# Performance work log

Hardware: AMD Instinct MI355X
Metric: run time of the kernel (lower is better)

The kernel has to match this reference:

```python
import jax, jax.numpy as jnp
import numpy as np

B, T, C, H = 4, 1024, 1024, 16
HS = C // H  # head_size = 64
EPS = 1e-5


def layer_norm(x, w, b):
    mu = jnp.mean(x, axis=-1, keepdims=True)
    var = jnp.mean(jnp.square(x - mu), axis=-1, keepdims=True)
    return (x - mu) * jax.lax.rsqrt(var + EPS) * w + b


def setup_inputs() -> dict:
    key = jax.random.key(0)
    ks = jax.random.split(key, 12)
    s = 0.02
    return {
        "x": jax.random.normal(ks[0], (B, T, C), jnp.float32),
        "ln1_w": jnp.ones((C,), jnp.float32),
        "ln1_b": jnp.zeros((C,), jnp.float32),
        "Wk": jax.random.normal(ks[1], (H, C, HS), jnp.float32) * s,
        "Wq": jax.random.normal(ks[2], (H, C, HS), jnp.float32) * s,
        "Wv": jax.random.normal(ks[3], (H, C, HS), jnp.float32) * s,
        "Wo": jax.random.normal(ks[4], (C, C), jnp.float32) * s,
        "bo": jnp.zeros((C,), jnp.float32),
        "ln2_w": jnp.ones((C,), jnp.float32),
        "ln2_b": jnp.zeros((C,), jnp.float32),
        "W1": jax.random.normal(ks[5], (C, 4 * C), jnp.float32) * s,
        "b1": jnp.zeros((4 * C,), jnp.float32),
        "prelu_a": jnp.asarray(0.25, jnp.float32),
        "W2": jax.random.normal(ks[6], (4 * C, C), jnp.float32) * s,
        "b2": jnp.zeros((C,), jnp.float32),
    }


def reference(x, ln1_w, ln1_b, Wk, Wq, Wv, Wo, bo, ln2_w, ln2_b, W1, b1, prelu_a, W2, b2):
    # --- self-attention branch (pre-LN) ---
    h = layer_norm(x, ln1_w, ln1_b)  # [B,T,C]
    k = jnp.einsum('btc,hcd->bhtd', h, Wk)
    q = jnp.einsum('btc,hcd->bhtd', h, Wq)
    v = jnp.einsum('btc,hcd->bhtd', h, Wv)
    # NOTE: source computes k @ q^T (not q @ k^T) scaled by n_embd**-0.5
    wei = jnp.einsum('bhtd,bhsd->bhts', k, q) * (C ** -0.5)  # [B,H,T,T]
    causal = jnp.tril(jnp.ones((T, T), bool))
    wei = jnp.where(causal, wei, -jnp.inf)
    wei = jax.nn.softmax(wei, axis=-1)
    out = jnp.einsum('bhts,bhsd->bthd', wei, v).reshape(B, T, C)
    out = out @ Wo + bo
    x = x + out
    # --- feed-forward branch (pre-LN) ---
    h2 = layer_norm(x, ln2_w, ln2_b)
    f = h2 @ W1 + b1
    f = jnp.where(f > 0, f, prelu_a * f)  # PReLU, single scalar param
    f = f @ W2 + b2
    return x + f
```

## Files before the change

### kernel.cpp

```cpp
#include <hip/hip_runtime.h>


typedef __bf16 bf16_t;
typedef __attribute__((ext_vector_type(8))) __bf16 bfx8;
typedef __attribute__((ext_vector_type(4))) __bf16 bfx4;
typedef __attribute__((ext_vector_type(4))) float f32x4;
typedef __attribute__((ext_vector_type(8))) unsigned short u16x8;
typedef unsigned int u32;

#define MFMA_BF16(a, b, c) __builtin_amdgcn_mfma_f32_16x16x32_bf16((a), (b), (c), 0, 0, 0)
#define GLOAD_LDS16(g, l)                                                     \
  __builtin_amdgcn_global_load_lds((__attribute__((address_space(1))) void*)(g), \
                                   (__attribute__((address_space(3))) void*)(l), 16, 0, 0)
#define SBAR() __builtin_amdgcn_sched_barrier(0)
#define VMW(N)                                          \
  asm volatile("s_waitcnt vmcnt(" #N ")" ::: "memory"); \
  __builtin_amdgcn_sched_barrier(0)

__device__ __forceinline__ int xcd_swz(int wg, int nb) {
  return (wg & 7) * (nb >> 3) + (wg >> 3);
}

__global__ __launch_bounds__(256) void ln_kernel(const float* __restrict__ x,
                                                 const float* __restrict__ w,
                                                 const float* __restrict__ b,
                                                 bf16_t* __restrict__ out) {
  const int row = blockIdx.x;
  const int tid = threadIdx.x;
  const float4 v = reinterpret_cast<const float4*>(x + (size_t)row * 1024)[tid];
  float s = v.x + v.y + v.z + v.w;
  float s2 = v.x * v.x + v.y * v.y + v.z * v.z + v.w * v.w;
#pragma unroll
  for (int off = 1; off < 64; off <<= 1) {
    s += __shfl_xor(s, off);
    s2 += __shfl_xor(s2, off);
  }
  __shared__ float red[8];
  const int wv = tid >> 6;
  if ((tid & 63) == 0) {
    red[wv] = s;
    red[4 + wv] = s2;
  }
  __syncthreads();
  s = red[0] + red[1] + red[2] + red[3];
  s2 = red[4] + red[5] + red[6] + red[7];
  const float mu = s * (1.0f / 1024.0f);
  const float rs = rsqrtf(s2 * (1.0f / 1024.0f) - mu * mu + 1e-5f);
  const float4 wv4 = reinterpret_cast<const float4*>(w)[tid];
  const float4 bv4 = reinterpret_cast<const float4*>(b)[tid];
  bfx4 o;
  o[0] = (bf16_t)((v.x - mu) * rs * wv4.x + bv4.x);
  o[1] = (bf16_t)((v.y - mu) * rs * wv4.y + bv4.y);
  o[2] = (bf16_t)((v.z - mu) * rs * wv4.z + bv4.z);
  o[3] = (bf16_t)((v.w - mu) * rs * wv4.w + bv4.w);
  reinterpret_cast<bfx4*>(out + (size_t)row * 1024)[tid] = o;
}

__device__ __forceinline__ void tc_body(const float* __restrict__ in,
                                        bf16_t* __restrict__ out, int K, int N, int k0,
                                        int n0, float (*tile)[65], int t) {
  const int rl = t >> 4, cl = (t & 15) * 4;
#pragma unroll
  for (int p = 0; p < 4; ++p) {
    const int r = p * 16 + rl;
    const float4 v = *reinterpret_cast<const float4*>(in + (size_t)(k0 + r) * N + n0 + cl);
    tile[r][cl] = v.x;
    tile[r][cl + 1] = v.y;
    tile[r][cl + 2] = v.z;
    tile[r][cl + 3] = v.w;
  }
  __syncthreads();
#pragma unroll
  for (int p = 0; p < 2; ++p) {
    const int idx = p * 256 + t;
    const int n = idx >> 3, kc = (idx & 7) * 8;
    bfx8 o;
#pragma unroll
    for (int i = 0; i < 8; ++i) o[i] = (bf16_t)tile[kc + i][n];
    *reinterpret_cast<bfx8*>(out + (size_t)(n0 + n) * K + k0 + kc) = o;
  }
}

__global__ __launch_bounds__(256) void transpose_cast(const float* __restrict__ in,
                                                      bf16_t* __restrict__ out, int K,
                                                      int N) {
  __shared__ float tile[64][65];
  tc_body(in, out, K, N, blockIdx.x * 64, blockIdx.y * 64, tile, threadIdx.x);
}

__global__ __launch_bounds__(256) void transpose_qkv(const float* __restrict__ Wq,
                                                     const float* __restrict__ Wk,
                                                     const float* __restrict__ Wv,
                                                     bf16_t* __restrict__ out) {
  __shared__ float tile[64][65];
  const int z = blockIdx.y;
  const int sel = z >> 4, h = z & 15;
  const float* in = ((sel == 0) ? Wq : (sel == 1) ? Wk : Wv) + h * 65536;
  bf16_t* o = out + (size_t)sel * 1048576 + h * 65536;
  tc_body(in, o, 1024, 64, blockIdx.x * 64, 0, tile, threadIdx.x);
}

enum { EPI_QKV = 0, EPI_WO = 1 };

template <int EPI, int BM, int BN, int NT>
__global__ __launch_bounds__(NT, 2) void gemm_bt(
    const bf16_t* __restrict__ A, const bf16_t* __restrict__ BT,
    const float* __restrict__ bias, const float* __restrict__ res,
    float* __restrict__ outf, bf16_t* __restrict__ ob0, bf16_t* __restrict__ ob1,
    bf16_t* __restrict__ ob2, int K, int N) {
  constexpr int WM = 2;
  constexpr int WN = NT / 64 / WM;
  constexpr int MF = BM / WM / 16;
  constexpr int NF = BN / WN / 16;
  constexpr int ACH = BM * 64 / (NT * 8);
  constexpr int BCH = BN * 64 / (NT * 8);
  constexpr int LOADS = ACH + BCH;
  static_assert(LOADS == 8 || LOADS == 6, "add a vmcnt case");
  __shared__ __align__(16) bf16_t sA[2][BM * 64];
  __shared__ __align__(16) bf16_t sB[2][BN * 64];
  const int tid = threadIdx.x;
  const int lane = tid & 63;
  const int w = tid >> 6;
  const int wr = w / WN, wc = w % WN;
  const int g = lane >> 4, l15 = lane & 15;
  const int nb = gridDim.x * gridDim.y;
  const int wg = blockIdx.y * gridDim.x + blockIdx.x;
  const int sg = xcd_swz(wg, nb);
  const int bx = sg % gridDim.x, by = sg / gridDim.x;
  const int row0 = bx * BM, col0 = by * BN;
  const int rowbase = row0 + wr * (BM / WM);
  const int colbase = wc * (BN / WN);

  f32x4 acc[MF][NF] = {};

  auto stage = [&](int k0, int buf) {
#pragma unroll
    for (int j = 0; j < ACH; ++j) {
      const int chunk = j * NT + tid;
      const int r = chunk >> 3, c = chunk & 7;
      GLOAD_LDS16(A + (size_t)(row0 + r) * K + k0 + ((c ^ (r & 7)) * 8),
                  sA[buf] + chunk * 8);
    }
#pragma unroll
    for (int j = 0; j < BCH; ++j) {
      const int chunk = j * NT + tid;
      const int r = chunk >> 3, c = chunk & 7;
      GLOAD_LDS16(BT + (size_t)(col0 + r) * K + k0 + ((c ^ (r & 7)) * 8),
                  sB[buf] + chunk * 8);
    }
  };

  stage(0, 0);
  const int nk = K >> 6;
  for (int t = 0; t < nk; ++t) {
    const int cur = t & 1;
    if (t + 1 < nk) {
      stage((t + 1) << 6, cur ^ 1);
      SBAR();
      if constexpr (LOADS == 8)
        asm volatile("s_waitcnt vmcnt(8)" ::: "memory");
      else
        asm volatile("s_waitcnt vmcnt(6)" ::: "memory");
    } else {
      SBAR();
      asm volatile("s_waitcnt vmcnt(0)" ::: "memory");
    }
    __builtin_amdgcn_s_barrier();
    SBAR();
    const bf16_t* __restrict__ pA = sA[cur];
    const bf16_t* __restrict__ pB = sB[cur];
#pragma unroll
    for (int kk = 0; kk < 2; ++kk) {
      bfx8 af[MF], bfr[NF];
#pragma unroll
      for (int m = 0; m < MF; ++m) {
        const int r = wr * (BM / WM) + m * 16 + l15;
        const int c = (kk * 4 + g) ^ (r & 7);
        af[m] = *reinterpret_cast<const bfx8*>(pA + r * 64 + c * 8);
      }
#pragma unroll
      for (int n = 0; n < NF; ++n) {
        const int r = colbase + n * 16 + l15;
        const int c = (kk * 4 + g) ^ (r & 7);
        bfr[n] = *reinterpret_cast<const bfx8*>(pB + r * 64 + c * 8);
      }
#pragma unroll
      for (int m = 0; m < MF; ++m)
#pragma unroll
        for (int n = 0; n < NF; ++n) acc[m][n] = MFMA_BF16(af[m], bfr[n], acc[m][n]);
    }
    SBAR();
    __builtin_amdgcn_s_barrier();
  }

#pragma unroll
  for (int m = 0; m < MF; ++m) {
#pragma unroll
    for (int n = 0; n < NF; ++n) {
#pragma unroll
      for (int j = 0; j < 4; ++j) {
        const int row = rowbase + m * 16 + (g << 2) + j;
        const int col = col0 + colbase + n * 16 + l15;
        const float v = acc[m][n][j];
        if (EPI == EPI_QKV) {
          const int sel = col >> 10;
          const int h = (col >> 6) & 15, d = col & 63;
          const int bb = row >> 10, t = row & 1023;
          bf16_t* dst = (sel == 0) ? ob0 : (sel == 1) ? ob1 : ob2;
          dst[((size_t)(bb * 16 + h) * 1024 + t) * 64 + d] = (bf16_t)v;
        } else {
          outf[(size_t)row * N + col] = v + bias[col] + res[(size_t)row * N + col];
        }
      }
    }
  }
}

__device__ __forceinline__ void stageA8(const bf16_t* __restrict__ A, int Ks, int row0,
                                        int k0, int mh, bf16_t* dst, int tid) {
#pragma unroll
  for (int g2 = 0; g2 < 2; ++g2) {
    const int band = g2 * 128 + mh * 64;
    const int row = band + (tid >> 3);
    GLOAD_LDS16(A + (size_t)(row0 + row) * Ks + k0 + (((tid & 7) ^ (row & 7)) * 8),
                dst + band * 64 + tid * 8);
  }
}

__device__ __forceinline__ void stageB8(const bf16_t* __restrict__ BT, int Ks, int col0,
                                        int k0, int nh, bf16_t* dst, int tid) {
#pragma unroll
  for (int g2 = 0; g2 < 2; ++g2) {
    const int rho = g2 * 64 + (tid >> 3);
    const int grow = (rho >> 5) * 64 + nh * 32 + (rho & 31);
    GLOAD_LDS16(BT + (size_t)(col0 + grow) * Ks + k0 + (((tid & 7) ^ (rho & 7)) * 8),
                dst + nh * 8192 + g2 * 4096 + tid * 8);
  }
}

template <int MH>
__device__ __forceinline__ void read_a8(const bf16_t* __restrict__ pA, int wr, int l15,
                                        int g, bfx8 (&af)[4][2]) {
#pragma unroll
  for (int i = 0; i < 4; ++i) {
    const int r = wr * 128 + (MH * 4 + i) * 16 + l15;
#pragma unroll
    for (int kk = 0; kk < 2; ++kk)
      af[i][kk] =
          *reinterpret_cast<const bfx8*>(pA + r * 64 + (((kk * 4 + g) ^ (r & 7)) * 8));
  }
}

template <int NH>
__device__ __forceinline__ void read_b8(const bf16_t* __restrict__ pB, int wc, int l15,
                                        int g, bfx8 (&bf)[2][2]) {
#pragma unroll
  for (int i = 0; i < 2; ++i) {
    const int rho = wc * 32 + i * 16 + l15;
#pragma unroll
    for (int kk = 0; kk < 2; ++kk)
      bf[i][kk] = *reinterpret_cast<const bfx8*>(pB + NH * 8192 + rho * 64 +
                                                 (((kk * 4 + g) ^ (rho & 7)) * 8));
  }
}

template <int MH, int NH>
__device__ __forceinline__ void mma16(const bfx8 (&af)[4][2], const bfx8 (&bf)[2][2],
                                      f32x4 (&acc)[8][4]) {
  __builtin_amdgcn_s_setprio(1);
#pragma unroll
  for (int i = 0; i < 4; ++i)
#pragma unroll
    for (int jn = 0; jn < 2; ++jn)
#pragma unroll
      for (int kk = 0; kk < 2; ++kk)
        acc[MH * 4 + i][NH * 2 + jn] =
            MFMA_BF16(af[i][kk], bf[jn][kk], acc[MH * 4 + i][NH * 2 + jn]);
  __builtin_amdgcn_s_setprio(0);
}

#define PHX(READS, STAGE, WAITC, MMA)                   \
  {                                                     \
    READS;                                              \
    STAGE;                                              \
    WAITC;                                              \
    __builtin_amdgcn_s_barrier();                       \
    asm volatile("s_waitcnt lgkmcnt(0)" ::: "memory");  \
    SBAR();                                             \
    MMA;                                                \
    SBAR();                                             \
    __builtin_amdgcn_s_barrier();                       \
  }

template <bool PRELU>
__global__ __launch_bounds__(512, 1) void gemm_8ph(
    const bf16_t* __restrict__ A, const bf16_t* __restrict__ BT,
    const float* __restrict__ bias, const float* __restrict__ prelu,
    bf16_t* __restrict__ outb, int Ks, int Klen, int N, size_t zstride, int nx,
    int nxy) {
  __shared__ __align__(16) bf16_t sA[2][256 * 64];
  __shared__ __align__(16) bf16_t sB[2][256 * 64];
  const int tid = threadIdx.x;
  const int lane = tid & 63;
  const int w = tid >> 6;
  const int wr = w >> 2, wc = w & 3;
  const int g = lane >> 4, l15 = lane & 15;
  const int sg = xcd_swz(blockIdx.x, gridDim.x);
  const int bz = sg / nxy;
  const int rxy = sg - bz * nxy;
  const int by = rxy / nx, bx = rxy - by * nx;
  const int row0 = bx * 256, col0 = by * 256;
  const int koff = bz * Klen;

  f32x4 acc[8][4] = {};
  bfx8 af[4][2];
  bfx8 b0[2][2], b1[2][2];

  stageA8(A, Ks, row0, koff, 0, sA[0], tid);
  stageB8(BT, Ks, col0, koff, 0, sB[0], tid);
  stageB8(BT, Ks, col0, koff, 1, sB[0], tid);
  stageA8(A, Ks, row0, koff, 1, sA[0], tid);
  stageA8(A, Ks, row0, koff + 64, 0, sA[1], tid);
  stageB8(BT, Ks, col0, koff + 64, 0, sB[1], tid);
  VMW(4);
  __builtin_amdgcn_s_barrier();

  const int nt = Klen >> 7;
  for (int j = 0; j < nt; ++j) {
    const bool more = (j + 1 < nt);
    const int ku1 = koff + ((2 * j + 1) << 6);
    const int k2 = koff + ((2 * j + 2) << 6);
    const int k3 = koff + ((2 * j + 3) << 6);
    PHX((read_a8<0>(sA[0], wr, l15, g, af), read_b8<0>(sB[0], wc, l15, g, b0)),
        stageB8(BT, Ks, col0, ku1, 1, sB[1], tid), ,
        (mma16<0, 0>(af, b0, acc)));
    PHX((read_b8<1>(sB[0], wc, l15, g, b1)),
        stageA8(A, Ks, row0, ku1, 1, sA[1], tid), ,
        (mma16<0, 1>(af, b1, acc)));
    PHX((read_a8<1>(sA[0], wr, l15, g, af)),
        if (more) stageA8(A, Ks, row0, k2, 0, sA[0], tid), ,
        (mma16<1, 0>(af, b0, acc)));
    PHX(, if (more) stageB8(BT, Ks, col0, k2, 0, sB[0], tid),
        if (more) { VMW(4); } else { VMW(0); },
        (mma16<1, 1>(af, b1, acc)));
    PHX((read_a8<0>(sA[1], wr, l15, g, af), read_b8<0>(sB[1], wc, l15, g, b0)),
        if (more) stageB8(BT, Ks, col0, k2, 1, sB[0], tid), ,
        (mma16<0, 0>(af, b0, acc)));
    PHX((read_b8<1>(sB[1], wc, l15, g, b1)),
        if (more) stageA8(A, Ks, row0, k2, 1, sA[0], tid), ,
        (mma16<0, 1>(af, b1, acc)));
    PHX((read_a8<1>(sA[1], wr, l15, g, af)),
        if (more) stageA8(A, Ks, row0, k3, 0, sA[1], tid), ,
        (mma16<1, 0>(af, b0, acc)));
    PHX(, if (more) stageB8(BT, Ks, col0, k3, 0, sB[1], tid),
        if (more) { VMW(4); },
        (mma16<1, 1>(af, b1, acc)));
  }

  bf16_t* o = outb + (size_t)bz * zstride;
  const float pa = PRELU ? prelu[0] : 0.0f;
#pragma unroll
  for (int m = 0; m < 8; ++m) {
#pragma unroll
    for (int n = 0; n < 4; ++n) {
#pragma unroll
      for (int j = 0; j < 4; ++j) {
        const int row = row0 + wr * 128 + m * 16 + (g << 2) + j;
        const int col = col0 + wc * 64 + n * 16 + l15;
        float t = acc[m][n][j];
        if (PRELU) {
          t += bias[col];
          t = (t > 0.0f) ? t : pa * t;
        }
        o[(size_t)row * N + col] = (bf16_t)t;
      }
    }
  }
}

__global__ __launch_bounds__(256) void reduce_mlp2(const bf16_t* __restrict__ part,
                                                   const float* __restrict__ b2,
                                                   float* __restrict__ out) {
  const int idx = (blockIdx.x * 256 + threadIdx.x) * 8;
  const int col = idx & 1023;
  float a[8];
  {
    const float4 o0 = *reinterpret_cast<const float4*>(out + idx);
    const float4 o1 = *reinterpret_cast<const float4*>(out + idx + 4);
    const float4 b0 = *reinterpret_cast<const float4*>(b2 + col);
    const float4 b1 = *reinterpret_cast<const float4*>(b2 + col + 4);
    a[0] = o0.x + b0.x; a[1] = o0.y + b0.y; a[2] = o0.z + b0.z; a[3] = o0.w + b0.w;
    a[4] = o1.x + b1.x; a[5] = o1.y + b1.y; a[6] = o1.z + b1.z; a[7] = o1.w + b1.w;
  }
#pragma unroll
  for (int s = 0; s < 4; ++s) {
    const u16x8 p = *reinterpret_cast<const u16x8*>(part + (size_t)s * 4194304 + idx);
#pragma unroll
    for (int i = 0; i < 8; ++i) a[i] += __uint_as_float((u32)p[i] << 16);
  }
  float4 r0{a[0], a[1], a[2], a[3]}, r1{a[4], a[5], a[6], a[7]};
  *reinterpret_cast<float4*>(out + idx) = r0;
  *reinterpret_cast<float4*>(out + idx + 4) = r1;
}

__global__ __launch_bounds__(256) void attn_kernel(const bf16_t* __restrict__ kproj,
                                                   const bf16_t* __restrict__ qproj,
                                                   const bf16_t* __restrict__ vproj,
                                                   bf16_t* __restrict__ att) {
  __shared__ __align__(16) bf16_t sK[2][64 * 64];
  __shared__ __align__(16) bf16_t sVt[2][64 * 64];
  __shared__ __align__(16) bf16_t sP[4][16 * 64];
  const int tid = threadIdx.x, lane = tid & 63, w = tid >> 6;
  const int g = lane >> 4, l15 = lane & 15;
  const int f = blockIdx.x;
  const int tb = 15 - ((f >> 3) >> 3);
  const int bh = (((f >> 3) & 7) << 3) + (f & 7);
  const size_t head = (size_t)bh * (1024 * 64);
  const int b = bh >> 4, h = bh & 15;
  const int vrow = 2 * (tid >> 3);
  const int vdb = tid & 7;
  const int t0 = tb * 64;
  const int nsb = tb + 1;

  bfx8 aq0, aq1;
  {
    const bf16_t* qrow = kproj + head + (size_t)(t0 + w * 16 + l15) * 64 + g * 8;
    aq0 = *reinterpret_cast<const bfx8*>(qrow);
    aq1 = *reinterpret_cast<const bfx8*>(qrow + 32);
  }

  {
#pragma unroll
    for (int j = 0; j < 2; ++j) {
      const int chunk = j * 256 + tid;
      const int r = chunk >> 3, c = chunk & 7;
      const int cs = c ^ (r & 7);
      GLOAD_LDS16(qproj + head + (size_t)r * 64 + cs * 8, sK[0] + chunk * 8);
    }
    const bf16_t* vp = vproj + head + (size_t)vrow * 64 + vdb * 8;
    const u16x8 v0 = *reinterpret_cast<const u16x8*>(vp);
    const u16x8 v1 = *reinterpret_cast<const u16x8*>(vp + 64);
#pragma unroll
    for (int i = 0; i < 8; ++i) {
      const int d = vdb * 8 + i;
      const int cc = ((vrow >> 3) ^ i ^ vdb) & 7;
      const u32 pk = ((u32)v1[i] << 16) | (u32)v0[i];
      *reinterpret_cast<u32*>(sVt[0] + d * 64 + cc * 8 + (vrow & 7)) = pk;
    }
  }
  __syncthreads();

  f32x4 accO[4] = {};
  float m2[4], lp[4];
#pragma unroll
  for (int j = 0; j < 4; ++j) {
    m2[j] = -1e30f;
    lp[j] = 0.0f;
  }

  for (int sb = 0; sb < nsb; ++sb) {
    const int cur = sb & 1;
    const bool pf = (sb + 1 < nsb);
    const bool diag = (sb == tb);
    u16x8 v0n, v1n;
    if (pf) {
      const int s0n = (sb + 1) * 64;
#pragma unroll
      for (int j = 0; j < 2; ++j) {
        const int chunk = j * 256 + tid;
        const int r = chunk >> 3, c = chunk & 7;
        const int cs = c ^ (r & 7);
        GLOAD_LDS16(qproj + head + (size_t)(s0n + r) * 64 + cs * 8, sK[cur ^ 1] + chunk * 8);
      }
      const bf16_t* vp = vproj + head + (size_t)(s0n + vrow) * 64 + vdb * 8;
      v0n = *reinterpret_cast<const u16x8*>(vp);
      v1n = *reinterpret_cast<const u16x8*>(vp + 64);
    }

    f32x4 accS[4] = {};
    const bf16_t* sKc = sK[cur];
#pragma unroll
    for (int kk = 0; kk < 2; ++kk) {
      const bfx8 aq = kk ? aq1 : aq0;
#pragma unroll
      for (int n = 0; n < 4; ++n) {
        const int r = n * 16 + l15;
        const int c = (kk * 4 + g) ^ (r & 7);
        const bfx8 bk = *reinterpret_cast<const bfx8*>(sKc + r * 64 + c * 8);
        accS[n] = MFMA_BF16(aq, bk, accS[n]);
      }
    }

    constexpr float SC = 0.04508056640625f;
    const int rbase = t0 + w * 16 + (g << 2);
    const int cbase = sb * 64 + l15;
    float rmx[4];
    float dmax = -3e38f;
#pragma unroll
    for (int j = 0; j < 4; ++j) {
      const int t = rbase + j;
      float mx = -1e30f;
      if (diag) {
#pragma unroll
        for (int n = 0; n < 4; ++n) {
          float v = accS[n][j] * SC;
          v = ((cbase + n * 16) <= t) ? v : -1e30f;
          accS[n][j] = v;
          mx = fmaxf(mx, v);
        }
      } else {
#pragma unroll
        for (int n = 0; n < 4; ++n) {
          const float v = accS[n][j] * SC;
          accS[n][j] = v;
          mx = fmaxf(mx, v);
        }
      }
      rmx[j] = mx;
      dmax = fmaxf(dmax, mx - m2[j]);
    }
    if (__any(dmax > 8.0f)) {
#pragma unroll
      for (int j = 0; j < 4; ++j) {
        float mx = rmx[j];
        mx = fmaxf(mx, __shfl_xor(mx, 1));
        mx = fmaxf(mx, __shfl_xor(mx, 2));
        mx = fmaxf(mx, __shfl_xor(mx, 4));
        mx = fmaxf(mx, __shfl_xor(mx, 8));
        const float mnew = fmaxf(m2[j], mx);
        const float al = __builtin_amdgcn_exp2f(m2[j] - mnew);
        m2[j] = mnew;
        lp[j] *= al;
#pragma unroll
        for (int n = 0; n < 4; ++n) accO[n][j] *= al;
      }
    }
#pragma unroll
    for (int j = 0; j < 4; ++j) {
      float s = 0.0f;
#pragma unroll
      for (int n = 0; n < 4; ++n) {
        const float p = __builtin_amdgcn_exp2f(accS[n][j] - m2[j]);
        accS[n][j] = p;
        s += p;
      }
      lp[j] += s;
    }

    bf16_t* sPw = sP[w];
#pragma unroll
    for (int n = 0; n < 4; ++n)
#pragma unroll
      for (int j = 0; j < 4; ++j) {
        const int r = (g << 2) + j;
        const int s = n * 16 + l15;
        const int cc = (s >> 3) ^ (r & 7);
        sPw[r * 64 + cc * 8 + (s & 7)] = (bf16_t)accS[n][j];
      }

    const bf16_t* sVc = sVt[cur];
#pragma unroll
    for (int kk = 0; kk < 2; ++kk) {
      bfx8 ap;
      {
        const int r = l15;
        const int c = (kk * 4 + g) ^ (r & 7);
        ap = *reinterpret_cast<const bfx8*>(sPw + r * 64 + c * 8);
      }
#pragma unroll
      for (int n = 0; n < 4; ++n) {
        const int d = n * 16 + l15;
        const int c = (kk * 4 + g) ^ (d & 7) ^ ((d >> 3) & 7);
        const bfx8 bv = *reinterpret_cast<const bfx8*>(sVc + d * 64 + c * 8);
        accO[n] = MFMA_BF16(ap, bv, accO[n]);
      }
    }

    if (pf) {
#pragma unroll
      for (int i = 0; i < 8; ++i) {
        const int d = vdb * 8 + i;
        const int cc = ((vrow >> 3) ^ i ^ vdb) & 7;
        const u32 pk = ((u32)v1n[i] << 16) | (u32)v0n[i];
        *reinterpret_cast<u32*>(sVt[cur ^ 1] + d * 64 + cc * 8 + (vrow & 7)) = pk;
      }
    }
    __syncthreads();
  }

#pragma unroll
  for (int j = 0; j < 4; ++j) {
    float l = lp[j];
    l += __shfl_xor(l, 1);
    l += __shfl_xor(l, 2);
    l += __shfl_xor(l, 4);
    l += __shfl_xor(l, 8);
    const float inv = 1.0f / l;
    const int t = t0 + w * 16 + (g << 2) + j;
#pragma unroll
    for (int n = 0; n < 4; ++n) {
      const int d = n * 16 + l15;
      att[((size_t)(b * 1024 + t)) * 1024 + h * 64 + d] = (bf16_t)(accO[n][j] * inv);
    }
  }
}

extern "C" void kernel_launch(void* const* d_in, const int* in_sizes, int n_in,
                              void* d_out, int out_size, void* d_ws, size_t ws_size,
                              hipStream_t stream) {
  (void)in_sizes; (void)n_in; (void)out_size; (void)ws_size;
  const float* x = (const float*)d_in[0];
  const float* ln1w = (const float*)d_in[1];
  const float* ln1b = (const float*)d_in[2];
  const float* Wk = (const float*)d_in[3];
  const float* Wq = (const float*)d_in[4];
  const float* Wv = (const float*)d_in[5];
  const float* Wo = (const float*)d_in[6];
  const float* bo = (const float*)d_in[7];
  const float* ln2w = (const float*)d_in[8];
  const float* ln2b = (const float*)d_in[9];
  const float* W1 = (const float*)d_in[10];
  const float* b1 = (const float*)d_in[11];
  const float* pa = (const float*)d_in[12];
  const float* W2 = (const float*)d_in[13];
  const float* b2 = (const float*)d_in[14];
  float* out = (float*)d_out;
  char* ws = (char*)d_ws;
  const size_t MB = 1ull << 20;
  bf16_t* h1 = (bf16_t*)(ws + 0 * MB);
  bf16_t* h2 = (bf16_t*)(ws + 8 * MB);
  bf16_t* qb = (bf16_t*)(ws + 16 * MB);
  bf16_t* kb = (bf16_t*)(ws + 24 * MB);
  bf16_t* vb = (bf16_t*)(ws + 32 * MB);
  bf16_t* attb = (bf16_t*)(ws + 40 * MB);
  bf16_t* fbuf = (bf16_t*)(ws + 48 * MB);
  bf16_t* part = (bf16_t*)(ws + 16 * MB);
  bf16_t* WqkvT = (bf16_t*)(ws + 80 * MB);
  bf16_t* WoT = (bf16_t*)(ws + 86 * MB);
  bf16_t* W1T = (bf16_t*)(ws + 88 * MB);
  bf16_t* W2T = (bf16_t*)(ws + 96 * MB);

  transpose_qkv<<<dim3(16, 48), 256, 0, stream>>>(Wq, Wk, Wv, WqkvT);
  transpose_cast<<<dim3(16, 16), 256, 0, stream>>>(Wo, WoT, 1024, 1024);
  transpose_cast<<<dim3(16, 64), 256, 0, stream>>>(W1, W1T, 1024, 4096);
  transpose_cast<<<dim3(64, 16), 256, 0, stream>>>(W2, W2T, 4096, 1024);

  ln_kernel<<<4096, 256, 0, stream>>>(x, ln1w, ln1b, h1);
  gemm_bt<EPI_QKV, 256, 256, 512><<<dim3(16, 12), 512, 0, stream>>>(
      h1, WqkvT, nullptr, nullptr, nullptr, qb, kb, vb, 1024, 3072);
  attn_kernel<<<1024, 256, 0, stream>>>(kb, qb, vb, attb);
  gemm_bt<EPI_WO, 64, 128, 256><<<dim3(64, 8), 256, 0, stream>>>(
      attb, WoT, bo, x, out, nullptr, nullptr, nullptr, 1024, 1024);
  ln_kernel<<<4096, 256, 0, stream>>>(out, ln2w, ln2b, h2);
  gemm_8ph<true><<<256, 512, 0, stream>>>(h2, W1T, b1, pa, fbuf, 1024, 1024, 4096, 0, 16,
                                          256);
  gemm_8ph<false><<<256, 512, 0, stream>>>(fbuf, W2T, nullptr, nullptr, part, 4096, 1024,
                                           1024, 4194304, 16, 64);
  reduce_mlp2<<<2048, 256, 0, stream>>>(part, b2, out);
}
```

Measured before the change: 203.4 us.

## Widen attention blocks to 128 queries and replace split-K MLP2 with single GEMM

The attention kernel now runs 512-thread blocks covering 128 query rows (8 waves), with the two 64-row halves sharing each K/V tile load. Waves whose row tile is already finished skip the compute for extra key blocks. This cuts redundant K/V loads and the block count, at the cost of idle waves on the diagonal block. The second MLP GEMM drops the split-K bf16 partial sums and separate reduce kernel. It uses gemm_bt with the EPI_WO epilogue, adding bias and residual in place, which removes a launch and the partial-buffer traffic but gives less parallelism for K=4096.

Measured after the change: 216.3 us. +6.3%, slower.

```diff
diff --git a/kernel.cpp b/kernel.cpp
--- a/kernel.cpp
+++ b/kernel.cpp
@@ -378,49 +378,25 @@
   }
 }
 
-__global__ __launch_bounds__(256) void reduce_mlp2(const bf16_t* __restrict__ part,
-                                                   const float* __restrict__ b2,
-                                                   float* __restrict__ out) {
-  const int idx = (blockIdx.x * 256 + threadIdx.x) * 8;
-  const int col = idx & 1023;
-  float a[8];
-  {
-    const float4 o0 = *reinterpret_cast<const float4*>(out + idx);
-    const float4 o1 = *reinterpret_cast<const float4*>(out + idx + 4);
-    const float4 b0 = *reinterpret_cast<const float4*>(b2 + col);
-    const float4 b1 = *reinterpret_cast<const float4*>(b2 + col + 4);
-    a[0] = o0.x + b0.x; a[1] = o0.y + b0.y; a[2] = o0.z + b0.z; a[3] = o0.w + b0.w;
-    a[4] = o1.x + b1.x; a[5] = o1.y + b1.y; a[6] = o1.z + b1.z; a[7] = o1.w + b1.w;
-  }
-#pragma unroll
-  for (int s = 0; s < 4; ++s) {
-    const u16x8 p = *reinterpret_cast<const u16x8*>(part + (size_t)s * 4194304 + idx);
-#pragma unroll
-    for (int i = 0; i < 8; ++i) a[i] += __uint_as_float((u32)p[i] << 16);
-  }
-  float4 r0{a[0], a[1], a[2], a[3]}, r1{a[4], a[5], a[6], a[7]};
-  *reinterpret_cast<float4*>(out + idx) = r0;
-  *reinterpret_cast<float4*>(out + idx + 4) = r1;
-}
-
-__global__ __launch_bounds__(256) void attn_kernel(const bf16_t* __restrict__ kproj,
+__global__ __launch_bounds__(512) void attn_kernel(const bf16_t* __restrict__ kproj,
                                                    const bf16_t* __restrict__ qproj,
                                                    const bf16_t* __restrict__ vproj,
                                                    bf16_t* __restrict__ att) {
   __shared__ __align__(16) bf16_t sK[2][64 * 64];
   __shared__ __align__(16) bf16_t sVt[2][64 * 64];
-  __shared__ __align__(16) bf16_t sP[4][16 * 64];
+  __shared__ __align__(16) bf16_t sP[8][16 * 64];
   const int tid = threadIdx.x, lane = tid & 63, w = tid >> 6;
   const int g = lane >> 4, l15 = lane & 15;
   const int f = blockIdx.x;
-  const int tb = 15 - ((f >> 3) >> 3);
-  const int bh = (((f >> 3) & 7) << 3) + (f & 7);
+  const int p = 7 - (f >> 6);
+  const int bh = f & 63;
   const size_t head = (size_t)bh * (1024 * 64);
   const int b = bh >> 4, h = bh & 15;
-  const int vrow = 2 * (tid >> 3);
+  const int vrow = tid >> 3;
   const int vdb = tid & 7;
-  const int t0 = tb * 64;
-  const int nsb = tb + 1;
+  const int t0 = p * 128;
+  const int nsb = 2 * p + 2;
+  const int wtb = 2 * p + (w >> 2);
 
   bfx8 aq0, aq1;
   {
@@ -430,22 +406,15 @@
   }
 
   {
-#pragma unroll
-    for (int j = 0; j < 2; ++j) {
-      const int chunk = j * 256 + tid;
-      const int r = chunk >> 3, c = chunk & 7;
-      const int cs = c ^ (r & 7);
-      GLOAD_LDS16(qproj + head + (size_t)r * 64 + cs * 8, sK[0] + chunk * 8);
-    }
-    const bf16_t* vp = vproj + head + (size_t)vrow * 64 + vdb * 8;
-    const u16x8 v0 = *reinterpret_cast<const u16x8*>(vp);
-    const u16x8 v1 = *reinterpret_cast<const u16x8*>(vp + 64);
+    const int r = tid >> 3, c = tid & 7;
+    GLOAD_LDS16(qproj + head + (size_t)r * 64 + ((c ^ (r & 7)) * 8), sK[0] + tid * 8);
+    const bfx8 v0 =
+        *reinterpret_cast<const bfx8*>(vproj + head + (size_t)vrow * 64 + vdb * 8);
 #pragma unroll
     for (int i = 0; i < 8; ++i) {
       const int d = vdb * 8 + i;
       const int cc = ((vrow >> 3) ^ i ^ vdb) & 7;
-      const u32 pk = ((u32)v1[i] << 16) | (u32)v0[i];
-      *reinterpret_cast<u32*>(sVt[0] + d * 64 + cc * 8 + (vrow & 7)) = pk;
+      sVt[0][d * 64 + cc * 8 + (vrow & 7)] = v0[i];
     }
   }
   __syncthreads();
@@ -461,118 +430,115 @@
   for (int sb = 0; sb < nsb; ++sb) {
     const int cur = sb & 1;
     const bool pf = (sb + 1 < nsb);
-    const bool diag = (sb == tb);
-    u16x8 v0n, v1n;
+    bfx8 v0n;
     if (pf) {
       const int s0n = (sb + 1) * 64;
-#pragma unroll
-      for (int j = 0; j < 2; ++j) {
-        const int chunk = j * 256 + tid;
-        const int r = chunk >> 3, c = chunk & 7;
-        const int cs = c ^ (r & 7);
-        GLOAD_LDS16(qproj + head + (size_t)(s0n + r) * 64 + cs * 8, sK[cur ^ 1] + chunk * 8);
-      }
-      const bf16_t* vp = vproj + head + (size_t)(s0n + vrow) * 64 + vdb * 8;
-      v0n = *reinterpret_cast<const u16x8*>(vp);
-      v1n = *reinterpret_cast<const u16x8*>(vp + 64);
-    }
-
-    f32x4 accS[4] = {};
-    const bf16_t* sKc = sK[cur];
-#pragma unroll
-    for (int kk = 0; kk < 2; ++kk) {
-      const bfx8 aq = kk ? aq1 : aq0;
-#pragma unroll
-      for (int n = 0; n < 4; ++n) {
-        const int r = n * 16 + l15;
-        const int c = (kk * 4 + g) ^ (r & 7);
-        const bfx8 bk = *reinterpret_cast<const bfx8*>(sKc + r * 64 + c * 8);
-        accS[n] = MFMA_BF16(aq, bk, accS[n]);
-      }
-    }
-
-    constexpr float SC = 0.04508056640625f;
-    const int rbase = t0 + w * 16 + (g << 2);
-    const int cbase = sb * 64 + l15;
-    float rmx[4];
-    float dmax = -3e38f;
-#pragma unroll
-    for (int j = 0; j < 4; ++j) {
-      const int t = rbase + j;
-      float mx = -1e30f;
-      if (diag) {
+      const int r = tid >> 3, c = tid & 7;
+      GLOAD_LDS16(qproj + head + (size_t)(s0n + r) * 64 + ((c ^ (r & 7)) * 8),
+                  sK[cur ^ 1] + tid * 8);
+      v0n = *reinterpret_cast<const bfx8*>(vproj + head + (size_t)(s0n + vrow) * 64 +
+                                           vdb * 8);
+    }
+
+    if (sb <= wtb) {
+      const bool diag = (sb == wtb);
+      f32x4 accS[4] = {};
+      const bf16_t* sKc = sK[cur];
+#pragma unroll
+      for (int kk = 0; kk < 2; ++kk) {
+        const bfx8 aq = kk ? aq1 : aq0;
 #pragma unroll
         for (int n = 0; n < 4; ++n) {
-          float v = accS[n][j] * SC;
-          v = ((cbase + n * 16) <= t) ? v : -1e30f;
-          accS[n][j] = v;
-          mx = fmaxf(mx, v);
-        }
-      } else {
+          const int r = n * 16 + l15;
+          const int c = (kk * 4 + g) ^ (r & 7);
+          const bfx8 bk = *reinterpret_cast<const bfx8*>(sKc + r * 64 + c * 8);
+          accS[n] = MFMA_BF16(aq, bk, accS[n]);
+        }
+      }
+
+      constexpr float SC = 0.04508056640625f;
+      const int rbase = t0 + w * 16 + (g << 2);
+      const int cbase = sb * 64 + l15;
+      float rmx[4];
+      float dmax = -3e38f;
+#pragma unroll
+      for (int j = 0; j < 4; ++j) {
+        const int t = rbase + j;
+        float mx = -1e30f;
+        if (diag) {
+#pragma unroll
+          for (int n = 0; n < 4; ++n) {
+            float v = accS[n][j] * SC;
+            v = ((cbase + n * 16) <= t) ? v : -1e30f;
+            accS[n][j] = v;
+            mx = fmaxf(mx, v);
+          }
+        } else {
+#pragma unroll
+          for (int n = 0; n < 4; ++n) {
+            const float v = accS[n][j] * SC;
+            accS[n][j] = v;
+            mx = fmaxf(mx, v);
+          }
+        }
+        rmx[j] = mx;
+        dmax = fmaxf(dmax, mx - m2[j]);
+      }
+      if (__any(dmax > 8.0f)) {
+#pragma unroll
+        for (int j = 0; j < 4; ++j) {
+          float mx = rmx[j];
+          mx = fmaxf(mx, __shfl_xor(mx, 1));
+          mx = fmaxf(mx, __shfl_xor(mx, 2));
+          mx = fmaxf(mx, __shfl_xor(mx, 4));
+          mx = fmaxf(mx, __shfl_xor(mx, 8));
+          const float mnew = fmaxf(m2[j], mx);
+          const float al = __builtin_amdgcn_exp2f(m2[j] - mnew);
+          m2[j] = mnew;
+          lp[j] *= al;
+#pragma unroll
+          for (int n = 0; n < 4; ++n) accO[n][j] *= al;
+        }
+      }
+#pragma unroll
+      for (int j = 0; j < 4; ++j) {
+        float s = 0.0f;
 #pragma unroll
         for (int n = 0; n < 4; ++n) {
-          const float v = accS[n][j] * SC;
-          accS[n][j] = v;
-          mx = fmaxf(mx, v);
-        }
-      }
-      rmx[j] = mx;
-      dmax = fmaxf(dmax, mx - m2[j]);
-    }
-    if (__any(dmax > 8.0f)) {
-#pragma unroll
-      for (int j = 0; j < 4; ++j) {
-        float mx = rmx[j];
-        mx = fmaxf(mx, __shfl_xor(mx, 1));
-        mx = fmaxf(mx, __shfl_xor(mx, 2));
-        mx = fmaxf(mx, __shfl_xor(mx, 4));
-        mx = fmaxf(mx, __shfl_xor(mx, 8));
-        const float mnew = fmaxf(m2[j], mx);
-        const float al = __builtin_amdgcn_exp2f(m2[j] - mnew);
-        m2[j] = mnew;
-        lp[j] *= al;
-#pragma unroll
-        for (int n = 0; n < 4; ++n) accO[n][j] *= al;
-      }
-    }
-#pragma unroll
-    for (int j = 0; j < 4; ++j) {
-      float s = 0.0f;
-#pragma unroll
-      for (int n = 0; n < 4; ++n) {
-        const float p = __builtin_amdgcn_exp2f(accS[n][j] - m2[j]);
-        accS[n][j] = p;
-        s += p;
-      }
-      lp[j] += s;
-    }
-
-    bf16_t* sPw = sP[w];
-#pragma unroll
-    for (int n = 0; n < 4; ++n)
-#pragma unroll
-      for (int j = 0; j < 4; ++j) {
-        const int r = (g << 2) + j;
-        const int s = n * 16 + l15;
-        const int cc = (s >> 3) ^ (r & 7);
-        sPw[r * 64 + cc * 8 + (s & 7)] = (bf16_t)accS[n][j];
-      }
-
-    const bf16_t* sVc = sVt[cur];
-#pragma unroll
-    for (int kk = 0; kk < 2; ++kk) {
-      bfx8 ap;
-      {
-        const int r = l15;
-        const int c = (kk * 4 + g) ^ (r & 7);
-        ap = *reinterpret_cast<const bfx8*>(sPw + r * 64 + c * 8);
-      }
-#pragma unroll
-      for (int n = 0; n < 4; ++n) {
-        const int d = n * 16 + l15;
-        const int c = (kk * 4 + g) ^ (d & 7) ^ ((d >> 3) & 7);
-        const bfx8 bv = *reinterpret_cast<const bfx8*>(sVc + d * 64 + c * 8);
-        accO[n] = MFMA_BF16(ap, bv, accO[n]);
+          const float pv = __builtin_amdgcn_exp2f(accS[n][j] - m2[j]);
+          accS[n][j] = pv;
+          s += pv;
+        }
+        lp[j] += s;
+      }
+
+      bf16_t* sPw = sP[w];
+#pragma unroll
+      for (int n = 0; n < 4; ++n)
+#pragma unroll
+        for (int j = 0; j < 4; ++j) {
+          const int r = (g << 2) + j;
+          const int s = n * 16 + l15;
+          const int cc = (s >> 3) ^ (r & 7);
+          sPw[r * 64 + cc * 8 + (s & 7)] = (bf16_t)accS[n][j];
+        }
+
+      const bf16_t* sVc = sVt[cur];
+#pragma unroll
+      for (int kk = 0; kk < 2; ++kk) {
+        bfx8 ap;
+        {
+          const int r = l15;
+          const int c = (kk * 4 + g) ^ (r & 7);
+          ap = *reinterpret_cast<const bfx8*>(sPw + r * 64 + c * 8);
+        }
+#pragma unroll
+        for (int n = 0; n < 4; ++n) {
+          const int d = n * 16 + l15;
+          const int c = (kk * 4 + g) ^ (d & 7) ^ ((d >> 3) & 7);
+          const bfx8 bv = *reinterpret_cast<const bfx8*>(sVc + d * 64 + c * 8);
+          accO[n] = MFMA_BF16(ap, bv, accO[n]);
+        }
       }
     }
 
@@ -581,8 +547,7 @@
       for (int i = 0; i < 8; ++i) {
         const int d = vdb * 8 + i;
         const int cc = ((vrow >> 3) ^ i ^ vdb) & 7;
-        const u32 pk = ((u32)v1n[i] << 16) | (u32)v0n[i];
-        *reinterpret_cast<u32*>(sVt[cur ^ 1] + d * 64 + cc * 8 + (vrow & 7)) = pk;
+        sVt[cur ^ 1][d * 64 + cc * 8 + (vrow & 7)] = v0n[i];
       }
     }
     __syncthreads();
@@ -634,7 +599,6 @@
   bf16_t* vb = (bf16_t*)(ws + 32 * MB);
   bf16_t* attb = (bf16_t*)(ws + 40 * MB);
   bf16_t* fbuf = (bf16_t*)(ws + 48 * MB);
-  bf16_t* part = (bf16_t*)(ws + 16 * MB);
   bf16_t* WqkvT = (bf16_t*)(ws + 80 * MB);
   bf16_t* WoT = (bf16_t*)(ws + 86 * MB);
   bf16_t* W1T = (bf16_t*)(ws + 88 * MB);
@@ -648,13 +612,12 @@
   ln_kernel<<<4096, 256, 0, stream>>>(x, ln1w, ln1b, h1);
   gemm_bt<EPI_QKV, 256, 256, 512><<<dim3(16, 12), 512, 0, stream>>>(
       h1, WqkvT, nullptr, nullptr, nullptr, qb, kb, vb, 1024, 3072);
-  attn_kernel<<<1024, 256, 0, stream>>>(kb, qb, vb, attb);
+  attn_kernel<<<512, 512, 0, stream>>>(kb, qb, vb, attb);
   gemm_bt<EPI_WO, 64, 128, 256><<<dim3(64, 8), 256, 0, stream>>>(
       attb, WoT, bo, x, out, nullptr, nullptr, nullptr, 1024, 1024);
   ln_kernel<<<4096, 256, 0, stream>>>(out, ln2w, ln2b, h2);
   gemm_8ph<true><<<256, 512, 0, stream>>>(h2, W1T, b1, pa, fbuf, 1024, 1024, 4096, 0, 16,
                                           256);
-  gemm_8ph<false><<<256, 512, 0, stream>>>(fbuf, W2T, nullptr, nullptr, part, 4096, 1024,
-                                           1024, 4194304, 16, 64);
-  reduce_mlp2<<<2048, 256, 0, stream>>>(part, b2, out);
-}
+  gemm_bt<EPI_WO, 64, 128, 256><<<dim3(64, 8), 256, 0, stream>>>(
+      fbuf, W2T, b2, out, out, nullptr, nullptr, nullptr, 4096, 1024);
+}
```

## Replace split-K MLP2 GEMM and reduction with single gemm_bt residual epilogue

Applied to the files above, without the earlier changes.

The second MLP GEMM, previously a split-K 8-phase kernel writing bf16 partials followed by a separate reduction kernel, now uses the existing gemm_bt kernel with the Wo-style epilogue (bias plus residual written to out) over K=4096. This removes the partial-buffer write/read traffic and one launch. It also adds a compile-time switch to disable the XCD block swizzle for the small-tile gemm_bt instances. Trade-off: the new path launches 512 blocks of 64x128 tiles over a long K loop, with no split-K parallelism, and reads and writes the same out buffer in place.

Result: slower. 208.9 us (+2.7%).

```diff
diff --git a/kernel.cpp b/kernel.cpp
--- a/kernel.cpp
+++ b/kernel.cpp
@@ -102,7 +102,7 @@
 
 enum { EPI_QKV = 0, EPI_WO = 1 };
 
-template <int EPI, int BM, int BN, int NT>
+template <int EPI, int BM, int BN, int NT, bool SWZ>
 __global__ __launch_bounds__(NT, 2) void gemm_bt(
     const bf16_t* __restrict__ A, const bf16_t* __restrict__ BT,
     const float* __restrict__ bias, const float* __restrict__ res,
@@ -123,10 +123,13 @@
   const int w = tid >> 6;
   const int wr = w / WN, wc = w % WN;
   const int g = lane >> 4, l15 = lane & 15;
-  const int nb = gridDim.x * gridDim.y;
-  const int wg = blockIdx.y * gridDim.x + blockIdx.x;
-  const int sg = xcd_swz(wg, nb);
-  const int bx = sg % gridDim.x, by = sg / gridDim.x;
+  int bx = blockIdx.x, by = blockIdx.y;
+  if (SWZ) {
+    const int nb = gridDim.x * gridDim.y;
+    const int sg = xcd_swz(blockIdx.y * gridDim.x + blockIdx.x, nb);
+    bx = sg % gridDim.x;
+    by = sg / gridDim.x;
+  }
   const int row0 = bx * BM, col0 = by * BN;
   const int rowbase = row0 + wr * (BM / WM);
   const int colbase = wc * (BN / WN);
@@ -378,31 +381,6 @@
   }
 }
 
-__global__ __launch_bounds__(256) void reduce_mlp2(const bf16_t* __restrict__ part,
-                                                   const float* __restrict__ b2,
-                                                   float* __restrict__ out) {
-  const int idx = (blockIdx.x * 256 + threadIdx.x) * 8;
-  const int col = idx & 1023;
-  float a[8];
-  {
-    const float4 o0 = *reinterpret_cast<const float4*>(out + idx);
-    const float4 o1 = *reinterpret_cast<const float4*>(out + idx + 4);
-    const float4 b0 = *reinterpret_cast<const float4*>(b2 + col);
-    const float4 b1 = *reinterpret_cast<const float4*>(b2 + col + 4);
-    a[0] = o0.x + b0.x; a[1] = o0.y + b0.y; a[2] = o0.z + b0.z; a[3] = o0.w + b0.w;
-    a[4] = o1.x + b1.x; a[5] = o1.y + b1.y; a[6] = o1.z + b1.z; a[7] = o1.w + b1.w;
-  }
-#pragma unroll
-  for (int s = 0; s < 4; ++s) {
-    const u16x8 p = *reinterpret_cast<const u16x8*>(part + (size_t)s * 4194304 + idx);
-#pragma unroll
-    for (int i = 0; i < 8; ++i) a[i] += __uint_as_float((u32)p[i] << 16);
-  }
-  float4 r0{a[0], a[1], a[2], a[3]}, r1{a[4], a[5], a[6], a[7]};
-  *reinterpret_cast<float4*>(out + idx) = r0;
-  *reinterpret_cast<float4*>(out + idx + 4) = r1;
-}
-
 __global__ __launch_bounds__(256) void attn_kernel(const bf16_t* __restrict__ kproj,
                                                    const bf16_t* __restrict__ qproj,
                                                    const bf16_t* __restrict__ vproj,
@@ -634,7 +612,6 @@
   bf16_t* vb = (bf16_t*)(ws + 32 * MB);
   bf16_t* attb = (bf16_t*)(ws + 40 * MB);
   bf16_t* fbuf = (bf16_t*)(ws + 48 * MB);
-  bf16_t* part = (bf16_t*)(ws + 16 * MB);
   bf16_t* WqkvT = (bf16_t*)(ws + 80 * MB);
   bf16_t* WoT = (bf16_t*)(ws + 86 * MB);
   bf16_t* W1T = (bf16_t*)(ws + 88 * MB);
@@ -646,15 +623,14 @@
   transpose_cast<<<dim3(64, 16), 256, 0, stream>>>(W2, W2T, 4096, 1024);
 
   ln_kernel<<<4096, 256, 0, stream>>>(x, ln1w, ln1b, h1);
-  gemm_bt<EPI_QKV, 256, 256, 512><<<dim3(16, 12), 512, 0, stream>>>(
+  gemm_bt<EPI_QKV, 256, 256, 512, true><<<dim3(16, 12), 512, 0, stream>>>(
       h1, WqkvT, nullptr, nullptr, nullptr, qb, kb, vb, 1024, 3072);
   attn_kernel<<<1024, 256, 0, stream>>>(kb, qb, vb, attb);
-  gemm_bt<EPI_WO, 64, 128, 256><<<dim3(64, 8), 256, 0, stream>>>(
+  gemm_bt<EPI_WO, 64, 128, 256, false><<<dim3(64, 8), 256, 0, stream>>>(
       attb, WoT, bo, x, out, nullptr, nullptr, nullptr, 1024, 1024);
   ln_kernel<<<4096, 256, 0, stream>>>(out, ln2w, ln2b, h2);
   gemm_8ph<true><<<256, 512, 0, stream>>>(h2, W1T, b1, pa, fbuf, 1024, 1024, 4096, 0, 16,
                                           256);
-  gemm_8ph<false><<<256, 512, 0, stream>>>(fbuf, W2T, nullptr, nullptr, part, 4096, 1024,
-                                           1024, 4194304, 16, 64);
-  reduce_mlp2<<<2048, 256, 0, stream>>>(part, b2, out);
-}
+  gemm_bt<EPI_WO, 64, 128, 256, false><<<dim3(64, 8), 256, 0, stream>>>(
+      fbuf, W2T, b2, out, out, nullptr, nullptr, nullptr, 4096, 1024);
+}
```
